# Optimization experiments

Measured on AMD Instinct MI355X. Metric: run time of the kernel, lower is better.

## Reference

```python
import jax, jax.numpy as jnp
import numpy as np

B, T, C = 2, 2048, 1024
H, D = 16, 64


def setup_inputs() -> dict:
    key = jax.random.key(0)
    ks = jax.random.split(key, 6)
    s = 0.02
    return {
        "x": jax.random.normal(ks[0], (B, T, C), dtype=jnp.float32),
        "W_qkv": jax.random.normal(ks[1], (3 * H * D, C), dtype=jnp.float32) * s,
        "b_qkv": jnp.zeros((3 * H * D,), dtype=jnp.float32),
        "W_proj": jax.random.normal(ks[2], (C, H * D), dtype=jnp.float32) * s,
        "b_proj": jnp.zeros((C,), dtype=jnp.float32),
        "sink_logit": jnp.zeros((H,), dtype=jnp.float32),
    }


def reference(x, W_qkv, b_qkv, W_proj, b_proj, sink_logit):
    Bx, Tx, Cx = x.shape
    qkv = x @ W_qkv.T + b_qkv  # (B,T,3*H*D)
    q, k, v = jnp.split(qkv, 3, axis=-1)
    # (B,T,H,D) -> (B,H,T,D)
    q = q.reshape(Bx, Tx, H, D).transpose(0, 2, 1, 3)
    k = k.reshape(Bx, Tx, H, D).transpose(0, 2, 1, 3)
    v = v.reshape(Bx, Tx, H, D).transpose(0, 2, 1, 3)
    scale = 1.0 / jnp.sqrt(jnp.asarray(D, dtype=x.dtype))
    scores = jnp.einsum("bhqd,bhkd->bhqk", q, k) * scale  # (B,H,T,T)
    neg_inf = jnp.finfo(x.dtype).min
    causal = jnp.tril(jnp.ones((Tx, Tx), dtype=bool))
    scores = jnp.where(causal[None, None], scores, neg_inf)
    # sink slot: k_sink = 0 so its logit is just the learnable sink bias
    sink = jnp.broadcast_to(sink_logit[None, :, None, None], (Bx, H, Tx, 1))
    logits = jnp.concatenate([sink.astype(scores.dtype), scores], axis=-1)  # (B,H,T,T+1)
    probs = jax.nn.softmax(logits, axis=-1)
    # v_sink is zero, so drop sink column in the value contraction
    out = jnp.einsum("bhqk,bhkd->bhqd", probs[..., 1:], v)
    y = out.transpose(0, 2, 1, 3).reshape(Bx, Tx, H * D)
    return y @ W_proj.T + b_proj
```

## Files before the change

kernel.cpp:

```cpp
#include <hip/hip_runtime.h>
#include <hip/hip_bf16.h>

#define Bb 2
#define Tt 2048
#define Cc 1024
#define Hh 16
#define Dd 64

typedef __bf16 bf8 __attribute__((ext_vector_type(8)));
typedef __bf16 bf4 __attribute__((ext_vector_type(4)));
typedef float f4 __attribute__((ext_vector_type(4)));

typedef __attribute__((address_space(3))) void lds_void;
typedef const __attribute__((address_space(1))) void g_void;

__device__ __forceinline__ void gload_lds16(const __bf16* g, __bf16* l) {
  __builtin_amdgcn_global_load_lds((g_void*)g, (lds_void*)l, 16, 0, 0);
}

__device__ __forceinline__ float ex2(float x) { return __builtin_amdgcn_exp2f(x); }

__global__ __launch_bounds__(256) void cvt3_kernel(
    const float* __restrict__ a, __bf16* __restrict__ oa, int na,
    const float* __restrict__ b, __bf16* __restrict__ ob, int nb,
    const float* __restrict__ c, __bf16* __restrict__ oc) {
  int gi = blockIdx.x * 256 + threadIdx.x;
  const int t0 = na >> 3, t1 = t0 + (nb >> 3);
  const float* src; __bf16* dst; int idx;
  if (gi < t0)      { src = a; dst = oa; idx = gi; }
  else if (gi < t1) { src = b; dst = ob; idx = gi - t0; }
  else              { src = c; dst = oc; idx = gi - t1; }
  const float* p = src + (size_t)idx * 8;
  float4 u = *(const float4*)p;
  float4 v = *(const float4*)(p + 4);
  bf8 r;
  r[0] = (__bf16)u.x; r[1] = (__bf16)u.y; r[2] = (__bf16)u.z; r[3] = (__bf16)u.w;
  r[4] = (__bf16)v.x; r[5] = (__bf16)v.y; r[6] = (__bf16)v.z; r[7] = (__bf16)v.w;
  *(bf8*)(dst + (size_t)idx * 8) = r;
}

__global__ __launch_bounds__(256) void gemm128_kernel(
    const __bf16* __restrict__ A, const __bf16* __restrict__ W,
    const float* __restrict__ bias, int K,
    __bf16* __restrict__ q_ws, __bf16* __restrict__ k_ws,
    __bf16* __restrict__ v_ws)
{
  const int tid = threadIdx.x;
  const int lane = tid & 63, wave = tid >> 6;
  const int lr = lane & 15, lq = lane >> 4;
  const int m_blk = blockIdx.y * 128, n_blk = blockIdx.x * 128;
  const int wm = (wave & 1) * 64, wn = (wave >> 1) * 64;

  __shared__ __align__(16) __bf16 As[128 * 32];
  __shared__ __align__(16) __bf16 Bs[128 * 32];
  __shared__ __align__(16) __bf16 Epi[4][64 * 72];

  const int srow = tid >> 2, scol = (tid & 3) * 8;
  const __bf16* ag0 = A + (size_t)(m_blk + srow) * K + scol;
  const __bf16* ag1 = A + (size_t)(m_blk + 64 + srow) * K + scol;
  const __bf16* bg0 = W + (size_t)(n_blk + srow) * K + scol;
  const __bf16* bg1 = W + (size_t)(n_blk + 64 + srow) * K + scol;
  __bf16* al0 = As + tid * 8;
  __bf16* al1 = As + 2048 + tid * 8;
  __bf16* bl0 = Bs + tid * 8;
  __bf16* bl1 = Bs + 2048 + tid * 8;

  f4 acc[4][4] = {};
  for (int k0 = 0; k0 < K; k0 += 32) {
    gload_lds16(ag0 + k0, al0);
    gload_lds16(ag1 + k0, al1);
    gload_lds16(bg0 + k0, bl0);
    gload_lds16(bg1 + k0, bl1);
    __syncthreads();

    bf8 af[4], bfr[4];
    #pragma unroll
    for (int i = 0; i < 4; ++i)
      af[i] = *(const bf8*)&As[(wm + i * 16 + lr) * 32 + lq * 8];
    #pragma unroll
    for (int j = 0; j < 4; ++j)
      bfr[j] = *(const bf8*)&Bs[(wn + j * 16 + lr) * 32 + lq * 8];
    #pragma unroll
    for (int i = 0; i < 4; ++i)
      #pragma unroll
      for (int j = 0; j < 4; ++j)
        acc[i][j] = __builtin_amdgcn_mfma_f32_16x16x32_bf16(af[i], bfr[j], acc[i][j], 0, 0, 0);
    __syncthreads();
  }

  const int col0 = n_blk + wn;
  const int which = col0 >> 10;
  const int b = m_blk >> 11;
  const int h = (col0 & 1023) >> 6;
  const size_t bh = (size_t)b * Hh + h;

  if (which == 2) {
    __bf16* E = Epi[wave];
    #pragma unroll
    for (int j = 0; j < 4; ++j) {
      float bv = bias[col0 + j * 16 + lr];
      #pragma unroll
      for (int i = 0; i < 4; ++i)
        #pragma unroll
        for (int r = 0; r < 4; ++r)
          E[(j * 16 + lr) * 72 + i * 16 + lq * 4 + r] = (__bf16)(acc[i][j][r] + bv);
    }
    asm volatile("s_waitcnt lgkmcnt(0)" ::: "memory");
    const int t0 = (m_blk + wm) & 2047;
    const int dd = lane >> 3, tl = (lane & 7) * 8;
    #pragma unroll
    for (int di = 0; di < 8; ++di) {
      int d = di * 8 + dd;
      bf8 vv = *(const bf8*)&E[d * 72 + tl];
      *(bf8*)&v_ws[(bh * Dd + d) * Tt + t0 + tl] = vv;
    }
  } else {
    __bf16* dst = (which == 0) ? q_ws : k_ws;
    const float scl = (which == 0) ? 0.18033688011112042f : 1.0f;
    #pragma unroll
    for (int i = 0; i < 4; ++i) {
      #pragma unroll
      for (int j = 0; j < 4; ++j) {
        #pragma unroll
        for (int r = 0; r < 4; ++r) {
          int row = m_blk + wm + i * 16 + lq * 4 + r;
          int col = col0 + j * 16 + lr;
          float val = (acc[i][j][r] + bias[col]) * scl;
          int d = col & 63, t = row & 2047;
          dst[(bh * Tt + t) * Dd + d] = (__bf16)val;
        }
      }
    }
  }
}

__global__ __launch_bounds__(256) void gemm64_kernel(
    const __bf16* __restrict__ A, const __bf16* __restrict__ W,
    const float* __restrict__ bias, int K, float* __restrict__ out, int ldo)
{
  const int tid = threadIdx.x;
  const int lane = tid & 63, wave = tid >> 6;
  const int lr = lane & 15, lq = lane >> 4;
  const int m_blk = blockIdx.y * 64, n_blk = blockIdx.x * 64;
  const int wm = (wave & 1) * 32, wn = (wave >> 1) * 32;

  __shared__ __align__(16) __bf16 As[64 * 32];
  __shared__ __align__(16) __bf16 Bs[64 * 32];

  const int srow = tid >> 2, scol = (tid & 3) * 8;
  const __bf16* ag = A + (size_t)(m_blk + srow) * K + scol;
  const __bf16* bg = W + (size_t)(n_blk + srow) * K + scol;
  __bf16* al = As + tid * 8;
  __bf16* bl = Bs + tid * 8;

  f4 acc[2][2] = {};
  for (int k0 = 0; k0 < K; k0 += 32) {
    gload_lds16(ag + k0, al);
    gload_lds16(bg + k0, bl);
    __syncthreads();

    bf8 af[2], bfr[2];
    #pragma unroll
    for (int i = 0; i < 2; ++i)
      af[i] = *(const bf8*)&As[(wm + i * 16 + lr) * 32 + lq * 8];
    #pragma unroll
    for (int j = 0; j < 2; ++j)
      bfr[j] = *(const bf8*)&Bs[(wn + j * 16 + lr) * 32 + lq * 8];
    #pragma unroll
    for (int i = 0; i < 2; ++i)
      #pragma unroll
      for (int j = 0; j < 2; ++j)
        acc[i][j] = __builtin_amdgcn_mfma_f32_16x16x32_bf16(af[i], bfr[j], acc[i][j], 0, 0, 0);
    __syncthreads();
  }

  #pragma unroll
  for (int i = 0; i < 2; ++i)
    #pragma unroll
    for (int j = 0; j < 2; ++j)
      #pragma unroll
      for (int r = 0; r < 4; ++r) {
        int row = m_blk + wm + i * 16 + lq * 4 + r;
        int col = n_blk + wn + j * 16 + lr;
        out[(size_t)row * ldo + col] = acc[i][j][r] + bias[col];
      }
}

__global__ __launch_bounds__(256) void attn_kernel(
    const __bf16* __restrict__ q_ws, const __bf16* __restrict__ k_ws,
    const __bf16* __restrict__ v_ws, const float* __restrict__ sink,
    __bf16* __restrict__ y_ws)
{
  int bi = blockIdx.x;
  int qt, bhi;
  if (bi < 256) { qt = 15 - (bi >> 5); bhi = bi & 31; }
  else          { qt = (bi - 256) >> 5; bhi = (bi - 256) & 31; }
  const int h = bhi & (Hh - 1);
  const int b = bhi >> 4;
  const int tid = threadIdx.x;
  const int lane = tid & 63, wave = tid >> 6;
  const int lr = lane & 15, lq = lane >> 4;

  __shared__ __align__(16) __bf16 KsU[3][64 * 64];
  __shared__ __align__(16) __bf16 VtU[3][64 * 64];
  __shared__ __align__(16) __bf16 PsU[4][2 * 16 * 64];

  const __bf16* qp = q_ws + (size_t)bhi * Tt * Dd;
  const __bf16* kp = k_ws + (size_t)bhi * Tt * Dd;
  const __bf16* vp = v_ws + (size_t)bhi * Dd * Tt;

  const int qbase = qt * 128;
  const int qlo = qbase + wave * 32;

  bf8 qf[2][2];
  #pragma unroll
  for (int qs = 0; qs < 2; ++qs) {
    const __bf16* qrow = qp + (size_t)(qlo + qs * 16 + lr) * Dd;
    qf[qs][0] = *(const bf8*)(qrow + lq * 8);
    qf[qs][1] = *(const bf8*)(qrow + 32 + lq * 8);
  }

  float rs[2] = {0.f, 0.f};
  f4 o_acc[2][4] = {};

  const int srow_lo = wave * 8 + (lane >> 3);
  const int sslot = lane & 7;
  const int nkt = 2 * qt + 2;

  auto stage = [&](int kt2, int bsel) {
    const int kbase2 = kt2 * 64;
    #pragma unroll
    for (int ii = 0; ii < 2; ++ii) {
      const int r = ii * 32 + srow_lo;
      const int cc = sslot ^ (r & 7);
      gload_lds16(kp + (size_t)(kbase2 + r) * Dd + cc * 8,
                  &KsU[bsel][ii * 2048 + wave * 512 + lane * 8]);
      gload_lds16(vp + (size_t)r * Tt + kbase2 + cc * 8,
                  &VtU[bsel][ii * 2048 + wave * 512 + lane * 8]);
    }
  };

  auto computeS = [&](const __bf16* Kb, f4 (&sA)[4][2]) {
    #pragma unroll
    for (int nt = 0; nt < 4; ++nt) {
      const int krow = nt * 16 + lr;
      const int x7 = krow & 7;
      bf8 kb0 = *(const bf8*)&Kb[krow * 64 + ((lq ^ x7) * 8)];
      bf8 kb1 = *(const bf8*)&Kb[krow * 64 + (((4 + lq) ^ x7) * 8)];
      #pragma unroll
      for (int qs = 0; qs < 2; ++qs) {
        f4 c = {};
        c = __builtin_amdgcn_mfma_f32_16x16x32_bf16(kb0, qf[qs][0], c, 0, 0, 0);
        c = __builtin_amdgcn_mfma_f32_16x16x32_bf16(kb1, qf[qs][1], c, 0, 0, 0);
        sA[nt][qs] = c;
      }
    }
  };

  f4 s_cur[4][2], s_next[4][2];

  stage(0, 0);
  __syncthreads();
  stage(1, 1);
  computeS(KsU[0], s_cur);

  for (int kt = 0; kt < nkt; ++kt) {
    __syncthreads();
    if (kt + 2 < nkt) stage(kt + 2, (kt + 2) % 3);

    if (kt + 1 < nkt && (kt + 1) * 64 <= qlo + 31)
      computeS(KsU[(kt + 1) % 3], s_next);

    const int kbase = kt * 64;
    if (kbase <= qlo + 31) {
      __bf16* Pw = PsU[wave];
      const bool diag = (kbase + 63 > qlo);
      if (diag) {
        #pragma unroll
        for (int nt = 0; nt < 4; ++nt)
          #pragma unroll
          for (int qs = 0; qs < 2; ++qs) {
            const int qg = qlo + qs * 16 + lr;
            const int kg = kbase + nt * 16 + lq * 4;
            bf4 pb;
            #pragma unroll
            for (int r = 0; r < 4; ++r) {
              float sv = (kg + r > qg) ? -1e30f : s_cur[nt][qs][r];
              float p = ex2(sv);
              rs[qs] += p;
              pb[r] = (__bf16)p;
            }
            const int G = (nt * 2 + (lq >> 1)) ^ (lr & 7);
            *(bf4*)&Pw[(qs * 16 + lr) * 64 + G * 8 + (lq & 1) * 4] = pb;
          }
      } else {
        #pragma unroll
        for (int nt = 0; nt < 4; ++nt)
          #pragma unroll
          for (int qs = 0; qs < 2; ++qs) {
            bf4 pb;
            #pragma unroll
            for (int r = 0; r < 4; ++r) {
              float p = ex2(s_cur[nt][qs][r]);
              rs[qs] += p;
              pb[r] = (__bf16)p;
            }
            const int G = (nt * 2 + (lq >> 1)) ^ (lr & 7);
            *(bf4*)&Pw[(qs * 16 + lr) * 64 + G * 8 + (lq & 1) * 4] = pb;
          }
      }
      asm volatile("s_waitcnt lgkmcnt(0)" ::: "memory");

      const __bf16* Vb = VtU[kt % 3];
      #pragma unroll
      for (int ks = 0; ks < 2; ++ks) {
        const int pg = ((ks * 4 + lq) ^ (lr & 7)) * 8;
        bf8 pa0 = *(const bf8*)&Pw[lr * 64 + pg];
        bf8 pa1 = *(const bf8*)&Pw[(16 + lr) * 64 + pg];
        #pragma unroll
        for (int dt = 0; dt < 4; ++dt) {
          const int vrow = dt * 16 + lr;
          bf8 vb = *(const bf8*)&Vb[vrow * 64 + (((ks * 4 + lq) ^ (vrow & 7)) * 8)];
          o_acc[0][dt] = __builtin_amdgcn_mfma_f32_16x16x32_bf16(pa0, vb, o_acc[0][dt], 0, 0, 0);
          o_acc[1][dt] = __builtin_amdgcn_mfma_f32_16x16x32_bf16(pa1, vb, o_acc[1][dt], 0, 0, 0);
        }
      }
    }

    #pragma unroll
    for (int nt = 0; nt < 4; ++nt)
      #pragma unroll
      for (int qs = 0; qs < 2; ++qs)
        s_cur[nt][qs] = s_next[nt][qs];
  }

  #pragma unroll
  for (int qs = 0; qs < 2; ++qs) {
    rs[qs] += __shfl_xor(rs[qs], 16, 64);
    rs[qs] += __shfl_xor(rs[qs], 32, 64);
  }
  const float snk = ex2(sink[h] * 1.44269504f);
  float inv0 = 1.0f / (rs[0] + snk);
  float inv1 = 1.0f / (rs[1] + snk);
  float invr[2][4];
  #pragma unroll
  for (int r = 0; r < 4; ++r) {
    invr[0][r] = __shfl(inv0, lq * 4 + r, 64);
    invr[1][r] = __shfl(inv1, lq * 4 + r, 64);
  }

  #pragma unroll
  for (int qs = 0; qs < 2; ++qs)
    #pragma unroll
    for (int dt = 0; dt < 4; ++dt)
      #pragma unroll
      for (int r = 0; r < 4; ++r) {
        int qrow = qbase + wave * 32 + qs * 16 + lq * 4 + r;
        y_ws[((size_t)b * Tt + qrow) * Cc + h * Dd + dt * 16 + lr] =
            (__bf16)(o_acc[qs][dt][r] * invr[qs][r]);
      }
}

extern "C" void kernel_launch(void* const* d_in, const int* in_sizes, int n_in,
                              void* d_out, int out_size, void* d_ws, size_t ws_size,
                              hipStream_t stream) {
  const float* x      = (const float*)d_in[0];
  const float* W_qkv  = (const float*)d_in[1];
  const float* b_qkv  = (const float*)d_in[2];
  const float* W_proj = (const float*)d_in[3];
  const float* b_proj = (const float*)d_in[4];
  const float* sinkp  = (const float*)d_in[5];
  float* out = (float*)d_out;

  const size_t n_x    = (size_t)Bb * Tt * Cc;
  const size_t n_wqkv = (size_t)3 * Hh * Dd * Cc;
  const size_t n_wprj = (size_t)Cc * Hh * Dd;
  const size_t nqkv   = (size_t)Bb * Hh * Tt * Dd;

  __bf16* xb     = (__bf16*)d_ws;
  __bf16* wqkvb  = xb + n_x;
  __bf16* wprojb = wqkvb + n_wqkv;
  __bf16* q_ws   = wprojb + n_wprj;
  __bf16* k_ws   = q_ws + nqkv;
  __bf16* v_ws   = k_ws + nqkv;
  __bf16* y_ws   = xb;

  dim3 blk(256);
  const int cvt_blocks = (int)((n_x + n_wqkv + n_wprj) / 8 / 256);
  cvt3_kernel<<<cvt_blocks, blk, 0, stream>>>(x, xb, (int)n_x,
                                              W_qkv, wqkvb, (int)n_wqkv,
                                              W_proj, wprojb);

  gemm128_kernel<<<dim3(3 * Cc / 128, Bb * Tt / 128), blk, 0, stream>>>(
      xb, wqkvb, b_qkv, Cc, q_ws, k_ws, v_ws);
  attn_kernel<<<dim3(512), blk, 0, stream>>>(q_ws, k_ws, v_ws, sinkp, y_ws);
  gemm64_kernel<<<dim3(Cc / 64, Bb * Tt / 64), blk, 0, stream>>>(
      y_ws, wprojb, b_proj, Hh * Dd, out, Cc);
}
```

Measured before the change: 186.0 us.

## Split attention query tile across eight waves of 16 rows each

The attention block grows from 4 to 8 waves, so each wave owns 16 query rows instead of 32 and the 128-row query tile per block stays the same. K/V staging is spread over 512 threads, so each thread issues one load per tile instead of two. This raises the wave count per block and cuts per-wave register use, which helps latency hiding. In exchange, each K/V fragment read from LDS now feeds only one MFMA instead of two, so LDS traffic per unit of compute doubles and causal imbalance between waves grows.

```diff
diff --git a/kernel.cpp b/kernel.cpp
--- a/kernel.cpp
+++ b/kernel.cpp
@@ -186,7 +186,7 @@
       }
 }
 
-__global__ __launch_bounds__(256) void attn_kernel(
+__global__ __launch_bounds__(512) void attn_kernel(
     const __bf16* __restrict__ q_ws, const __bf16* __restrict__ k_ws,
     const __bf16* __restrict__ v_ws, const float* __restrict__ sink,
     __bf16* __restrict__ y_ws)
@@ -203,61 +203,53 @@
 
   __shared__ __align__(16) __bf16 KsU[3][64 * 64];
   __shared__ __align__(16) __bf16 VtU[3][64 * 64];
-  __shared__ __align__(16) __bf16 PsU[4][2 * 16 * 64];
+  __shared__ __align__(16) __bf16 PsU[8][16 * 64];
 
   const __bf16* qp = q_ws + (size_t)bhi * Tt * Dd;
   const __bf16* kp = k_ws + (size_t)bhi * Tt * Dd;
   const __bf16* vp = v_ws + (size_t)bhi * Dd * Tt;
 
   const int qbase = qt * 128;
-  const int qlo = qbase + wave * 32;
-
-  bf8 qf[2][2];
-  #pragma unroll
-  for (int qs = 0; qs < 2; ++qs) {
-    const __bf16* qrow = qp + (size_t)(qlo + qs * 16 + lr) * Dd;
-    qf[qs][0] = *(const bf8*)(qrow + lq * 8);
-    qf[qs][1] = *(const bf8*)(qrow + 32 + lq * 8);
-  }
-
-  float rs[2] = {0.f, 0.f};
-  f4 o_acc[2][4] = {};
-
-  const int srow_lo = wave * 8 + (lane >> 3);
-  const int sslot = lane & 7;
+  const int qlo = qbase + wave * 16;
+
+  bf8 qf[2];
+  {
+    const __bf16* qrow = qp + (size_t)(qlo + lr) * Dd;
+    qf[0] = *(const bf8*)(qrow + lq * 8);
+    qf[1] = *(const bf8*)(qrow + 32 + lq * 8);
+  }
+
+  float rs = 0.f;
+  f4 o_acc[4] = {};
+
+  const int srow_g = tid >> 3;
+  const int sslot = tid & 7;
   const int nkt = 2 * qt + 2;
 
   auto stage = [&](int kt2, int bsel) {
     const int kbase2 = kt2 * 64;
-    #pragma unroll
-    for (int ii = 0; ii < 2; ++ii) {
-      const int r = ii * 32 + srow_lo;
-      const int cc = sslot ^ (r & 7);
-      gload_lds16(kp + (size_t)(kbase2 + r) * Dd + cc * 8,
-                  &KsU[bsel][ii * 2048 + wave * 512 + lane * 8]);
-      gload_lds16(vp + (size_t)r * Tt + kbase2 + cc * 8,
-                  &VtU[bsel][ii * 2048 + wave * 512 + lane * 8]);
-    }
+    const int cc = sslot ^ (srow_g & 7);
+    gload_lds16(kp + (size_t)(kbase2 + srow_g) * Dd + cc * 8,
+                &KsU[bsel][wave * 512 + lane * 8]);
+    gload_lds16(vp + (size_t)srow_g * Tt + kbase2 + cc * 8,
+                &VtU[bsel][wave * 512 + lane * 8]);
   };
 
-  auto computeS = [&](const __bf16* Kb, f4 (&sA)[4][2]) {
+  auto computeS = [&](const __bf16* Kb, f4 (&sA)[4]) {
     #pragma unroll
     for (int nt = 0; nt < 4; ++nt) {
       const int krow = nt * 16 + lr;
       const int x7 = krow & 7;
       bf8 kb0 = *(const bf8*)&Kb[krow * 64 + ((lq ^ x7) * 8)];
       bf8 kb1 = *(const bf8*)&Kb[krow * 64 + (((4 + lq) ^ x7) * 8)];
-      #pragma unroll
-      for (int qs = 0; qs < 2; ++qs) {
-        f4 c = {};
-        c = __builtin_amdgcn_mfma_f32_16x16x32_bf16(kb0, qf[qs][0], c, 0, 0, 0);
-        c = __builtin_amdgcn_mfma_f32_16x16x32_bf16(kb1, qf[qs][1], c, 0, 0, 0);
-        sA[nt][qs] = c;
-      }
+      f4 c = {};
+      c = __builtin_amdgcn_mfma_f32_16x16x32_bf16(kb0, qf[0], c, 0, 0, 0);
+      c = __builtin_amdgcn_mfma_f32_16x16x32_bf16(kb1, qf[1], c, 0, 0, 0);
+      sA[nt] = c;
     }
   };
 
-  f4 s_cur[4][2], s_next[4][2];
+  f4 s_cur[4], s_next[4];
 
   stage(0, 0);
   __syncthreads();
@@ -268,46 +260,42 @@
     __syncthreads();
     if (kt + 2 < nkt) stage(kt + 2, (kt + 2) % 3);
 
-    if (kt + 1 < nkt && (kt + 1) * 64 <= qlo + 31)
+    if (kt + 1 < nkt && (kt + 1) * 64 <= qlo + 15)
       computeS(KsU[(kt + 1) % 3], s_next);
 
     const int kbase = kt * 64;
-    if (kbase <= qlo + 31) {
+    if (kbase <= qlo + 15) {
       __bf16* Pw = PsU[wave];
       const bool diag = (kbase + 63 > qlo);
       if (diag) {
         #pragma unroll
-        for (int nt = 0; nt < 4; ++nt)
+        for (int nt = 0; nt < 4; ++nt) {
+          const int qg = qlo + lr;
+          const int kg = kbase + nt * 16 + lq * 4;
+          bf4 pb;
           #pragma unroll
-          for (int qs = 0; qs < 2; ++qs) {
-            const int qg = qlo + qs * 16 + lr;
-            const int kg = kbase + nt * 16 + lq * 4;
-            bf4 pb;
-            #pragma unroll
-            for (int r = 0; r < 4; ++r) {
-              float sv = (kg + r > qg) ? -1e30f : s_cur[nt][qs][r];
-              float p = ex2(sv);
-              rs[qs] += p;
-              pb[r] = (__bf16)p;
-            }
-            const int G = (nt * 2 + (lq >> 1)) ^ (lr & 7);
-            *(bf4*)&Pw[(qs * 16 + lr) * 64 + G * 8 + (lq & 1) * 4] = pb;
+          for (int r = 0; r < 4; ++r) {
+            float sv = (kg + r > qg) ? -1e30f : s_cur[nt][r];
+            float p = ex2(sv);
+            rs += p;
+            pb[r] = (__bf16)p;
           }
+          const int G = (nt * 2 + (lq >> 1)) ^ (lr & 7);
+          *(bf4*)&Pw[lr * 64 + G * 8 + (lq & 1) * 4] = pb;
+        }
       } else {
         #pragma unroll
-        for (int nt = 0; nt < 4; ++nt)
+        for (int nt = 0; nt < 4; ++nt) {
+          bf4 pb;
           #pragma unroll
-          for (int qs = 0; qs < 2; ++qs) {
-            bf4 pb;
-            #pragma unroll
-            for (int r = 0; r < 4; ++r) {
-              float p = ex2(s_cur[nt][qs][r]);
-              rs[qs] += p;
-              pb[r] = (__bf16)p;
-            }
-            const int G = (nt * 2 + (lq >> 1)) ^ (lr & 7);
-            *(bf4*)&Pw[(qs * 16 + lr) * 64 + G * 8 + (lq & 1) * 4] = pb;
+          for (int r = 0; r < 4; ++r) {
+            float p = ex2(s_cur[nt][r]);
+            rs += p;
+            pb[r] = (__bf16)p;
           }
+          const int G = (nt * 2 + (lq >> 1)) ^ (lr & 7);
+          *(bf4*)&Pw[lr * 64 + G * 8 + (lq & 1) * 4] = pb;
+        }
       }
       asm volatile("s_waitcnt lgkmcnt(0)" ::: "memory");
 
@@ -315,50 +303,38 @@
       #pragma unroll
       for (int ks = 0; ks < 2; ++ks) {
         const int pg = ((ks * 4 + lq) ^ (lr & 7)) * 8;
-        bf8 pa0 = *(const bf8*)&Pw[lr * 64 + pg];
-        bf8 pa1 = *(const bf8*)&Pw[(16 + lr) * 64 + pg];
+        bf8 pa = *(const bf8*)&Pw[lr * 64 + pg];
         #pragma unroll
         for (int dt = 0; dt < 4; ++dt) {
           const int vrow = dt * 16 + lr;
           bf8 vb = *(const bf8*)&Vb[vrow * 64 + (((ks * 4 + lq) ^ (vrow & 7)) * 8)];
-          o_acc[0][dt] = __builtin_amdgcn_mfma_f32_16x16x32_bf16(pa0, vb, o_acc[0][dt], 0, 0, 0);
-          o_acc[1][dt] = __builtin_amdgcn_mfma_f32_16x16x32_bf16(pa1, vb, o_acc[1][dt], 0, 0, 0);
+          o_acc[dt] = __builtin_amdgcn_mfma_f32_16x16x32_bf16(pa, vb, o_acc[dt], 0, 0, 0);
         }
       }
     }
 
     #pragma unroll
     for (int nt = 0; nt < 4; ++nt)
-      #pragma unroll
-      for (int qs = 0; qs < 2; ++qs)
-        s_cur[nt][qs] = s_next[nt][qs];
-  }
-
+      s_cur[nt] = s_next[nt];
+  }
+
+  rs += __shfl_xor(rs, 16, 64);
+  rs += __shfl_xor(rs, 32, 64);
+  const float snk = ex2(sink[h] * 1.44269504f);
+  float inv = 1.0f / (rs + snk);
+  float invr[4];
   #pragma unroll
-  for (int qs = 0; qs < 2; ++qs) {
-    rs[qs] += __shfl_xor(rs[qs], 16, 64);
-    rs[qs] += __shfl_xor(rs[qs], 32, 64);
-  }
-  const float snk = ex2(sink[h] * 1.44269504f);
-  float inv0 = 1.0f / (rs[0] + snk);
-  float inv1 = 1.0f / (rs[1] + snk);
-  float invr[2][4];
+  for (int r = 0; r < 4; ++r)
+    invr[r] = __shfl(inv, lq * 4 + r, 64);
+
   #pragma unroll
-  for (int r = 0; r < 4; ++r) {
-    invr[0][r] = __shfl(inv0, lq * 4 + r, 64);
-    invr[1][r] = __shfl(inv1, lq * 4 + r, 64);
-  }
-
-  #pragma unroll
-  for (int qs = 0; qs < 2; ++qs)
-    #pragma unroll
-    for (int dt = 0; dt < 4; ++dt)
-      #pragma unroll
-      for (int r = 0; r < 4; ++r) {
-        int qrow = qbase + wave * 32 + qs * 16 + lq * 4 + r;
-        y_ws[((size_t)b * Tt + qrow) * Cc + h * Dd + dt * 16 + lr] =
-            (__bf16)(o_acc[qs][dt][r] * invr[qs][r]);
-      }
+  for (int dt = 0; dt < 4; ++dt)
+    #pragma unroll
+    for (int r = 0; r < 4; ++r) {
+      int qrow = qlo + lq * 4 + r;
+      y_ws[((size_t)b * Tt + qrow) * Cc + h * Dd + dt * 16 + lr] =
+          (__bf16)(o_acc[dt][r] * invr[r]);
+    }
 }
 
 extern "C" void kernel_launch(void* const* d_in, const int* in_sizes, int n_in,
@@ -393,7 +369,7 @@
 
   gemm128_kernel<<<dim3(3 * Cc / 128, Bb * Tt / 128), blk, 0, stream>>>(
       xb, wqkvb, b_qkv, Cc, q_ws, k_ws, v_ws);
-  attn_kernel<<<dim3(512), blk, 0, stream>>>(q_ws, k_ws, v_ws, sinkp, y_ws);
+  attn_kernel<<<dim3(512), dim3(512), 0, stream>>>(q_ws, k_ws, v_ws, sinkp, y_ws);
   gemm64_kernel<<<dim3(Cc / 64, Bb * Tt / 64), blk, 0, stream>>>(
       y_ws, wprojb, b_proj, Hh * Dd, out, Cc);
 }
```

Result: faster. 180.3 us (-3.1%).
